# Performance work log

Measured on AMD Instinct MI355X. Metric: run time of the kernel, lower is better.

The kernel has to match this reference:

```python
import jax, jax.numpy as jnp
import numpy as np

B = 131072  # batch of states
D = 32      # input/hidden width (hardcoded in Policy)
L = 40      # number of hidden layers

def setup_inputs() -> dict:
    key = jax.random.key(0)
    k1, k2, k3, k4, k5 = jax.random.split(key, 5)
    scale = 1.0 / np.sqrt(D)  # ~ torch Linear init scale
    return {
        "state": jax.random.normal(k1, (B, D), dtype=jnp.float32),
        "W_hidden": jax.random.normal(k2, (L, D, D), dtype=jnp.float32) * scale,
        "b_hidden": jax.random.normal(k3, (L, D), dtype=jnp.float32) * scale,
        "W_out": jax.random.normal(k4, (1, D), dtype=jnp.float32) * scale,
        "b_out": jax.random.normal(k5, (1,), dtype=jnp.float32) * scale,
    }

def reference(state, W_hidden, b_hidden, W_out, b_out):
    # torch Linear: y = x @ W.T + b, with W of shape [out, in].
    def layer(x, wb):
        w, b = wb
        return jax.nn.relu(jnp.einsum('bi,oi->bo', x, w) + b), None
    x, _ = jax.lax.scan(layer, state, (W_hidden, b_hidden))
    # final Linear(32, 1), no activation
    return jnp.einsum('bi,oi->bo', x, W_out) + b_out  # [B, 1]
```

## Files before the change

kernel.cpp:

```cpp
#include <hip/hip_runtime.h>


#define NB 131072
#define DD 32
#define NL 40
#define WTAB_BYTES ((NL + 1) * 4 * 64 * 16)

typedef short bf16x8 __attribute__((ext_vector_type(8)));
typedef float f32x4 __attribute__((ext_vector_type(4)));

union Frag { int4 q; int i[4]; bf16x8 v; };
union BFrag { float4 q; f32x4 v; };

__device__ inline unsigned f2bf(float f) {
  unsigned u = __float_as_uint(f);
  return (u + 0x7fffu + ((u >> 16) & 1u)) >> 16;
}
__device__ inline float bf2f(unsigned s) { return __int_as_float((int)(s << 16)); }

__global__ __launch_bounds__(64) void build_tables(
    const float* __restrict__ Wh, const float* __restrict__ bh,
    const float* __restrict__ Wout, const float* __restrict__ bout,
    int4* __restrict__ wtab, float4* __restrict__ btab) {
  const int l = blockIdx.x;
  const int lane = threadIdx.x;
  const int m = lane & 15, g = lane >> 4;
  for (int p = 0; p < 4; ++p) {
    const int row = (p & 1) ? (16 + m) : m;
    const bool lopart = (p >= 2);
    int wds[4];
    for (int w = 0; w < 4; ++w) {
      unsigned wd = 0;
      for (int e = 0; e < 2; ++e) {
        const int j = 2 * w + e;
        const int k = (j < 4) ? (4 * g + j) : (16 + 4 * g + (j - 4));
        float v;
        if (l < NL) v = Wh[(l * 32 + row) * 32 + k];
        else        v = (row == 0) ? Wout[k] : 0.f;
        unsigned hi = f2bf(v);
        unsigned val = lopart ? f2bf(v - bf2f(hi)) : hi;
        wd |= val << (16 * e);
      }
      wds[w] = (int)wd;
    }
    wtab[(l * 4 + p) * 64 + lane] = make_int4(wds[0], wds[1], wds[2], wds[3]);
  }
  for (int a = 0; a < 2; ++a) {
    float bv[4];
    for (int r = 0; r < 4; ++r) {
      const int row = 16 * a + 4 * g + r;
      bv[r] = (l < NL) ? bh[l * 32 + row] : ((row == 0) ? bout[0] : 0.f);
    }
    btab[(l * 2 + a) * 64 + lane] = make_float4(bv[0], bv[1], bv[2], bv[3]);
  }
}

__device__ inline void split2(float a, float b, int& hi, int& lo) {
  const unsigned ia = __float_as_uint(a), ib = __float_as_uint(b);
  hi = (int)__builtin_amdgcn_perm(ia, ib, 0x03020706u);
  const float ha = __int_as_float((int)(ia & 0xffff0000u));
  const float hb = __int_as_float((int)(ib & 0xffff0000u));
  const float la = a - ha, lb = b - hb;
  lo = (int)__builtin_amdgcn_perm(__float_as_uint(la), __float_as_uint(lb),
                                  0x03020706u);
}

#define MFMA16(A, B, C) __builtin_amdgcn_mfma_f32_16x16x32_bf16((A), (B), (C), 0, 0, 0)

__global__ __launch_bounds__(256, 4) void policy_mfma(
    const float* __restrict__ state, const int4* __restrict__ wtab,
    const float4* __restrict__ btab, float* __restrict__ out) {
  const int lane = threadIdx.x & 63;
  const int wid = (int)((blockIdx.x * blockDim.x + threadIdx.x) >> 6);
  const int n = lane & 15, g = lane >> 4;
  const int bbase = wid * 32;

  Frag bhi[2], blo[2];
#pragma unroll
  for (int t = 0; t < 2; ++t) {
    const float* xr = state + (size_t)(bbase + 16 * t + n) * DD;
    float4 xa = *(const float4*)(xr + 4 * g);
    float4 xc = *(const float4*)(xr + 16 + 4 * g);
    split2(xa.x, xa.y, bhi[t].i[0], blo[t].i[0]);
    split2(xa.z, xa.w, bhi[t].i[1], blo[t].i[1]);
    split2(xc.x, xc.y, bhi[t].i[2], blo[t].i[2]);
    split2(xc.z, xc.w, bhi[t].i[3], blo[t].i[3]);
  }

  const int4* wp = wtab + lane;
  const float4* bp = btab + lane;

#pragma unroll
  for (int l = 0; l < NL; ++l) {
    Frag w0h, w1h, w0l, w1l;
    w0h.q = wp[l * 256 + 0];
    w1h.q = wp[l * 256 + 64];
    w0l.q = wp[l * 256 + 128];
    w1l.q = wp[l * 256 + 192];
    BFrag c0, c1;
    c0.q = bp[l * 128 + 0];
    c1.q = bp[l * 128 + 64];

    f32x4 a00 = MFMA16(w0h.v, bhi[0].v, c0.v);
    f32x4 a01 = MFMA16(w1h.v, bhi[0].v, c1.v);
    f32x4 a10 = MFMA16(w0h.v, bhi[1].v, c0.v);
    f32x4 a11 = MFMA16(w1h.v, bhi[1].v, c1.v);
    a00 = MFMA16(w0l.v, bhi[0].v, a00);
    a01 = MFMA16(w1l.v, bhi[0].v, a01);
    a10 = MFMA16(w0l.v, bhi[1].v, a10);
    a11 = MFMA16(w1l.v, bhi[1].v, a11);
    a00 = MFMA16(w0h.v, blo[0].v, a00);
    a01 = MFMA16(w1h.v, blo[0].v, a01);
    a10 = MFMA16(w0h.v, blo[1].v, a10);
    a11 = MFMA16(w1h.v, blo[1].v, a11);

    split2(fmaxf(a00[0], 0.f), fmaxf(a00[1], 0.f), bhi[0].i[0], blo[0].i[0]);
    split2(fmaxf(a00[2], 0.f), fmaxf(a00[3], 0.f), bhi[0].i[1], blo[0].i[1]);
    split2(fmaxf(a01[0], 0.f), fmaxf(a01[1], 0.f), bhi[0].i[2], blo[0].i[2]);
    split2(fmaxf(a01[2], 0.f), fmaxf(a01[3], 0.f), bhi[0].i[3], blo[0].i[3]);
    split2(fmaxf(a10[0], 0.f), fmaxf(a10[1], 0.f), bhi[1].i[0], blo[1].i[0]);
    split2(fmaxf(a10[2], 0.f), fmaxf(a10[3], 0.f), bhi[1].i[1], blo[1].i[1]);
    split2(fmaxf(a11[0], 0.f), fmaxf(a11[1], 0.f), bhi[1].i[2], blo[1].i[2]);
    split2(fmaxf(a11[2], 0.f), fmaxf(a11[3], 0.f), bhi[1].i[3], blo[1].i[3]);
  }

  float res0, res1;
  {
    Frag w0h, w0l;
    w0h.q = wp[NL * 256 + 0];
    w0l.q = wp[NL * 256 + 128];
    BFrag c0;
    c0.q = bp[NL * 128 + 0];
    f32x4 a00 = MFMA16(w0h.v, bhi[0].v, c0.v);
    f32x4 a10 = MFMA16(w0h.v, bhi[1].v, c0.v);
    a00 = MFMA16(w0l.v, bhi[0].v, a00);
    a10 = MFMA16(w0l.v, bhi[1].v, a10);
    a00 = MFMA16(w0h.v, blo[0].v, a00);
    a10 = MFMA16(w0h.v, blo[1].v, a10);
    res0 = a00[0];
    res1 = a10[0];
  }

  if (lane < 16) {
    out[bbase + n] = res0;
    out[bbase + 16 + n] = res1;
  }
}

extern "C" void kernel_launch(void* const* d_in, const int* in_sizes, int n_in,
                              void* d_out, int out_size, void* d_ws, size_t ws_size,
                              hipStream_t stream) {
  const float* state = (const float*)d_in[0];
  const float* Wh    = (const float*)d_in[1];
  const float* bh    = (const float*)d_in[2];
  const float* Wout  = (const float*)d_in[3];
  const float* bout  = (const float*)d_in[4];
  float* out = (float*)d_out;

  int4* wtab = (int4*)d_ws;
  float4* btab = (float4*)((char*)d_ws + WTAB_BYTES);

  build_tables<<<NL + 1, 64, 0, stream>>>(Wh, bh, Wout, bout, wtab, btab);

  policy_mfma<<<(NB / 32) * 64 / 256, 256, 0, stream>>>(state, wtab, btab, out);
}
```

Baseline: 48.26 us.

## Stage per-layer weight and bias tables in LDS with 1024-thread blocks

Each block now cooperatively copies the bias table and the bf16 hi/lo weight fragments for the first 38 layers into shared memory, then runs those layers from LDS. The last two layers and the output layer still read from global memory. The launch changes to 256 blocks of 1024 threads, one block per CU using nearly all of its LDS. This targets the repeated per-layer global/L2 weight loads on the critical path, at the cost of a serialized prologue copy, a barrier and a fixed occupancy of 16 waves per CU.

```diff
diff --git a/kernel.cpp b/kernel.cpp
--- a/kernel.cpp
+++ b/kernel.cpp
@@ -4,7 +4,11 @@
 #define NB 131072
 #define DD 32
 #define NL 40
+#define BIAS_BYTES ((NL + 1) * 32 * 4)
+#define WTAB_OFF   BIAS_BYTES
 #define WTAB_BYTES ((NL + 1) * 4 * 64 * 16)
+#define LDS_LAYERS 38
+#define LDS_BYTES  (BIAS_BYTES + LDS_LAYERS * 4096)
 
 typedef short bf16x8 __attribute__((ext_vector_type(8)));
 typedef float f32x4 __attribute__((ext_vector_type(4)));
@@ -21,10 +25,12 @@
 __global__ __launch_bounds__(64) void build_tables(
     const float* __restrict__ Wh, const float* __restrict__ bh,
     const float* __restrict__ Wout, const float* __restrict__ bout,
-    int4* __restrict__ wtab, float4* __restrict__ btab) {
+    char* __restrict__ ws) {
   const int l = blockIdx.x;
   const int lane = threadIdx.x;
   const int m = lane & 15, g = lane >> 4;
+  int4* wtab = (int4*)(ws + WTAB_OFF);
+  float* bc = (float*)ws;
   for (int p = 0; p < 4; ++p) {
     const int row = (p & 1) ? (16 + m) : m;
     const bool lopart = (p >= 2);
@@ -45,13 +51,9 @@
     }
     wtab[(l * 4 + p) * 64 + lane] = make_int4(wds[0], wds[1], wds[2], wds[3]);
   }
-  for (int a = 0; a < 2; ++a) {
-    float bv[4];
-    for (int r = 0; r < 4; ++r) {
-      const int row = 16 * a + 4 * g + r;
-      bv[r] = (l < NL) ? bh[l * 32 + row] : ((row == 0) ? bout[0] : 0.f);
-    }
-    btab[(l * 2 + a) * 64 + lane] = make_float4(bv[0], bv[1], bv[2], bv[3]);
+  if (lane < 32) {
+    float bv = (l < NL) ? bh[l * 32 + lane] : ((lane == 0) ? bout[0] : 0.f);
+    bc[l * 32 + lane] = bv;
   }
 }
 
@@ -67,12 +69,21 @@
 
 #define MFMA16(A, B, C) __builtin_amdgcn_mfma_f32_16x16x32_bf16((A), (B), (C), 0, 0, 0)
 
-__global__ __launch_bounds__(256, 4) void policy_mfma(
-    const float* __restrict__ state, const int4* __restrict__ wtab,
-    const float4* __restrict__ btab, float* __restrict__ out) {
-  const int lane = threadIdx.x & 63;
-  const int wid = (int)((blockIdx.x * blockDim.x + threadIdx.x) >> 6);
+__global__ __launch_bounds__(1024, 4) void policy_mfma(
+    const float* __restrict__ state, const char* __restrict__ tab,
+    float* __restrict__ out) {
+  extern __shared__ char smem[];
+  const int tid = threadIdx.x;
+  const int lane = tid & 63;
   const int n = lane & 15, g = lane >> 4;
+
+  {
+    const int4* src = (const int4*)tab;
+    int4* dst = (int4*)smem;
+    for (int i = tid; i < LDS_BYTES / 16; i += 1024) dst[i] = src[i];
+  }
+
+  const int wid = blockIdx.x * 16 + (tid >> 6);
   const int bbase = wid * 32;
 
   Frag bhi[2], blo[2];
@@ -87,19 +98,21 @@
     split2(xc.z, xc.w, bhi[t].i[3], blo[t].i[3]);
   }
 
-  const int4* wp = wtab + lane;
-  const float4* bp = btab + lane;
+  __syncthreads();
 
-#pragma unroll
-  for (int l = 0; l < NL; ++l) {
+  const int4* lw = (const int4*)(smem + WTAB_OFF);
+  const float* lb = (const float*)smem;
+  const int4* gw = (const int4*)(tab + WTAB_OFF);
+
+  auto layer = [&](int l, const int4* __restrict__ WP) {
     Frag w0h, w1h, w0l, w1l;
-    w0h.q = wp[l * 256 + 0];
-    w1h.q = wp[l * 256 + 64];
-    w0l.q = wp[l * 256 + 128];
-    w1l.q = wp[l * 256 + 192];
+    w0h.q = WP[l * 256 + lane];
+    w1h.q = WP[l * 256 + 64 + lane];
+    w0l.q = WP[l * 256 + 128 + lane];
+    w1l.q = WP[l * 256 + 192 + lane];
     BFrag c0, c1;
-    c0.q = bp[l * 128 + 0];
-    c1.q = bp[l * 128 + 64];
+    c0.q = *(const float4*)(lb + l * 32 + 4 * g);
+    c1.q = *(const float4*)(lb + l * 32 + 16 + 4 * g);
 
     f32x4 a00 = MFMA16(w0h.v, bhi[0].v, c0.v);
     f32x4 a01 = MFMA16(w1h.v, bhi[0].v, c1.v);
@@ -122,15 +135,20 @@
     split2(fmaxf(a10[2], 0.f), fmaxf(a10[3], 0.f), bhi[1].i[1], blo[1].i[1]);
     split2(fmaxf(a11[0], 0.f), fmaxf(a11[1], 0.f), bhi[1].i[2], blo[1].i[2]);
     split2(fmaxf(a11[2], 0.f), fmaxf(a11[3], 0.f), bhi[1].i[3], blo[1].i[3]);
-  }
+  };
+
+#pragma unroll
+  for (int l = 0; l < LDS_LAYERS; ++l) layer(l, lw);
+#pragma unroll
+  for (int l = LDS_LAYERS; l < NL; ++l) layer(l, gw);
 
   float res0, res1;
   {
     Frag w0h, w0l;
-    w0h.q = wp[NL * 256 + 0];
-    w0l.q = wp[NL * 256 + 128];
+    w0h.q = gw[NL * 256 + lane];
+    w0l.q = gw[NL * 256 + 128 + lane];
     BFrag c0;
-    c0.q = bp[NL * 128 + 0];
+    c0.q = *(const float4*)(lb + NL * 32 + 4 * g);
     f32x4 a00 = MFMA16(w0h.v, bhi[0].v, c0.v);
     f32x4 a10 = MFMA16(w0h.v, bhi[1].v, c0.v);
     a00 = MFMA16(w0l.v, bhi[0].v, a00);
@@ -157,10 +175,7 @@
   const float* bout  = (const float*)d_in[4];
   float* out = (float*)d_out;
 
-  int4* wtab = (int4*)d_ws;
-  float4* btab = (float4*)((char*)d_ws + WTAB_BYTES);
+  build_tables<<<NL + 1, 64, 0, stream>>>(Wh, bh, Wout, bout, (char*)d_ws);
 
-  build_tables<<<NL + 1, 64, 0, stream>>>(Wh, bh, Wout, bout, wtab, btab);
-
-  policy_mfma<<<(NB / 32) * 64 / 256, 256, 0, stream>>>(state, wtab, btab, out);
+  policy_mfma<<<256, 1024, LDS_BYTES, stream>>>(state, (const char*)d_ws, out);
 }
```

After: 44.56 us. 1.08x faster.
